# Optimization experiments

Hardware: AMD Instinct MI355X
Metric: run time of the kernel (lower is better)

## Reference

```python
import jax, jax.numpy as jnp
import numpy as np

B, S, D, E, H, K = 2, 2048, 1024, 8, 4096, 2


def setup_inputs() -> dict:
    key = jax.random.key(0)
    ks = jax.random.split(key, 7)
    sd = 1.0 / np.sqrt(D)
    sh = 1.0 / np.sqrt(H)
    return {
        "x": jax.random.normal(ks[0], (B, S, D), dtype=jnp.float32),
        "router_w": jax.random.uniform(ks[1], (D, E), jnp.float32, -sd, sd),
        "router_b": jnp.zeros((E,), jnp.float32),
        "w1": jax.random.uniform(ks[2], (E, D, H), jnp.float32, -sd, sd),
        "b1": jnp.zeros((E, H), jnp.float32),
        "w2": jax.random.uniform(ks[3], (E, H, D), jnp.float32, -sh, sh),
        "b2": jnp.zeros((E, D), jnp.float32),
    }


def reference(x, router_w, router_b, w1, b1, w2, b2):
    # Router: softmax over experts, then top-k and renormalize
    router_logits = jnp.einsum("bsd,de->bse", x, router_w) + router_b
    router_probs = jax.nn.softmax(router_logits, axis=-1)
    top_k_probs, top_k_indices = jax.lax.top_k(router_probs, K)  # [B,S,K]
    top_k_probs = top_k_probs / jnp.sum(top_k_probs, axis=-1, keepdims=True)

    # Dense all-expert FFN (Block assumed: Linear -> GELU -> Linear)
    h = jax.nn.gelu(jnp.einsum("bsd,edh->bseh", x, w1) + b1)  # [B,S,E,H]
    expert_outputs = jnp.einsum("bseh,ehd->bsed", h, w2) + b2  # [B,S,E,D]

    # Gather top-k experts per token and combine with renormalized probs
    idx = top_k_indices[..., None]  # [B,S,K,1]
    selected = jnp.take_along_axis(expert_outputs, idx, axis=2)  # [B,S,K,D]
    return jnp.sum(selected * top_k_probs[..., None], axis=2)  # [B,S,D]
```

## Files before the change

kernel.cpp:

```cpp
#include <hip/hip_runtime.h>
#include <hip/hip_bf16.h>

#define TOK   4096
#define DDIM  1024
#define NEXP  8
#define HDIM  4096
#define KSEL  2
#define NPAIR (TOK * KSEL)
#define NSPLIT 4

typedef __attribute__((ext_vector_type(8))) _Float16 f16x8;
typedef __attribute__((ext_vector_type(4))) _Float16 f16x4;
typedef __attribute__((ext_vector_type(4))) float    f32x4;

__device__ __forceinline__ void gload16(const void* g, void* l) {
  __builtin_amdgcn_global_load_lds((const __attribute__((address_space(1))) void*)g,
                                   (__attribute__((address_space(3))) void*)l, 16, 0, 0);
}

__device__ __forceinline__ float gelu_tanh(float u) {
  float inner = 0.7978845608028654f * (u + 0.044715f * u * u * u);
  float t2 = __expf(2.f * inner);
  return u - u / (t2 + 1.f);
}

__global__ __launch_bounds__(256) void k_router(const float* __restrict__ x,
    const float* __restrict__ rw, const float* __restrict__ rb,
    int* __restrict__ tidx, float* __restrict__ tw,
    _Float16* __restrict__ xb) {
  const int t    = blockIdx.x * 4 + (threadIdx.x >> 6);
  const int lane = threadIdx.x & 63;
  const float* xr = x + (size_t)t * DDIM;
  _Float16*   xbr = xb + (size_t)t * DDIM;
  float acc[NEXP];
#pragma unroll
  for (int e = 0; e < NEXP; ++e) acc[e] = 0.f;
  for (int d0 = lane * 4; d0 < DDIM; d0 += 256) {
    const float4 xv = *(const float4*)(xr + d0);
    f16x4 hx;
    hx[0] = (_Float16)xv.x; hx[1] = (_Float16)xv.y;
    hx[2] = (_Float16)xv.z; hx[3] = (_Float16)xv.w;
    *(f16x4*)(xbr + d0) = hx;
#pragma unroll
    for (int i = 0; i < 4; ++i) {
      const float xs = (&xv.x)[i];
      const float4 r0 = *(const float4*)(rw + (size_t)(d0 + i) * NEXP);
      const float4 r1 = *(const float4*)(rw + (size_t)(d0 + i) * NEXP + 4);
      acc[0] += xs * r0.x; acc[1] += xs * r0.y; acc[2] += xs * r0.z; acc[3] += xs * r0.w;
      acc[4] += xs * r1.x; acc[5] += xs * r1.y; acc[6] += xs * r1.z; acc[7] += xs * r1.w;
    }
  }
#pragma unroll
  for (int e = 0; e < NEXP; ++e) {
    float v = acc[e];
#pragma unroll
    for (int s = 32; s; s >>= 1) v += __shfl_xor(v, s, 64);
    acc[e] = v;
  }
  if (lane == 0) {
    float lg[NEXP];
#pragma unroll
    for (int e = 0; e < NEXP; ++e) lg[e] = acc[e] + rb[e];
    int i0 = 0;
#pragma unroll
    for (int e = 1; e < NEXP; ++e) if (lg[e] > lg[i0]) i0 = e;
    int i1 = -1; float best = -3.4e38f;
#pragma unroll
    for (int e = 0; e < NEXP; ++e) {
      if (e == i0) continue;
      if (lg[e] > best) { best = lg[e]; i1 = e; }
    }
    float w0 = 1.f / (1.f + expf(lg[i1] - lg[i0]));
    tidx[t * 2]     = i0;  tidx[t * 2 + 1] = i1;
    tw[t * 2]       = w0;  tw[t * 2 + 1]   = 1.f - w0;
  }
}

__global__ __launch_bounds__(1024) void k_scan(const int* __restrict__ tidx,
                       const float* __restrict__ tw,
                       int* __restrict__ offs,
                       int* __restrict__ row_token, float* __restrict__ row_w,
                       int* __restrict__ inv) {
  __shared__ int hist[NEXP];
  __shared__ int soff[NEXP + 1];
  __shared__ int scur[NEXP];
  if (threadIdx.x < NEXP) hist[threadIdx.x] = 0;
  __syncthreads();
  const int lane = threadIdx.x & 63;
  int e_loc[NPAIR / 1024];
#pragma unroll
  for (int it = 0; it < NPAIR / 1024; ++it) {
    const int p = it * 1024 + threadIdx.x;
    const int e = tidx[p];
    e_loc[it] = e;
#pragma unroll
    for (int ee = 0; ee < NEXP; ++ee) {
      unsigned long long m = __ballot(e == ee);
      if (m && lane == 0) atomicAdd(&hist[ee], __popcll(m));
    }
  }
  __syncthreads();
  if (threadIdx.x == 0) {
    int run = 0;
    for (int e = 0; e < NEXP; ++e) { soff[e] = run; scur[e] = run; run += hist[e]; }
    soff[NEXP] = run;
    for (int e = 0; e <= NEXP; ++e) offs[e] = soff[e];
  }
  __syncthreads();
#pragma unroll
  for (int it = 0; it < NPAIR / 1024; ++it) {
    const int p = it * 1024 + threadIdx.x;
    const int e = e_loc[it];
    int pos = 0;
#pragma unroll
    for (int ee = 0; ee < NEXP; ++ee) {
      unsigned long long m = __ballot(e == ee);
      if (!m) continue;
      int base = 0;
      if (lane == 0) base = atomicAdd(&scur[ee], __popcll(m));
      base = __shfl(base, 0, 64);
      if (e == ee) pos = base + __popcll(m & ((1ull << lane) - 1ull));
    }
    row_token[pos] = p >> 1;
    row_w[pos]     = tw[p];
    inv[p]         = pos;
  }
}

__global__ __launch_bounds__(256) void k_transpose(const float* __restrict__ in,
    _Float16* __restrict__ out, int Rr, int Cc) {
  __shared__ _Float16 tile[64][72];
  const size_t esz = (size_t)Rr * Cc;
  const float* ip = in + esz * blockIdx.z;
  _Float16*    op = out + esz * blockIdx.z;
  const int i0 = blockIdx.y * 64;
  const int j0 = blockIdx.x * 64;
  const int tx = threadIdx.x & 15, ty = threadIdx.x >> 4;
#pragma unroll
  for (int rr = 0; rr < 4; ++rr) {
    int r = ty + rr * 16;
    float4 v = *(const float4*)(ip + (size_t)(i0 + r) * Cc + j0 + tx * 4);
    tile[r][tx * 4 + 0] = (_Float16)v.x;
    tile[r][tx * 4 + 1] = (_Float16)v.y;
    tile[r][tx * 4 + 2] = (_Float16)v.z;
    tile[r][tx * 4 + 3] = (_Float16)v.w;
  }
  __syncthreads();
#pragma unroll
  for (int cc = 0; cc < 4; ++cc) {
    int c = ty + cc * 16;
    f16x4 o;
#pragma unroll
    for (int k = 0; k < 4; ++k) o[k] = tile[tx * 4 + k][c];
    *(f16x4*)(op + (size_t)(j0 + c) * Rr + i0 + tx * 4) = o;
  }
}

#define BM 128
#define BN 128
#define BKK 32


__global__ __launch_bounds__(256) void k_gemm1(
    const _Float16* __restrict__ xb,
    const _Float16* __restrict__ w1t,
    const float* __restrict__ b1,
    const int* __restrict__ offs,
    const int* __restrict__ row_token,
    _Float16* __restrict__ hbuf) {
  const int e    = blockIdx.z;
  const int off0 = offs[e];
  const int ne   = offs[e + 1] - off0;
  const int m0   = blockIdx.y * BM;
  if (m0 >= ne) return;
  const int n0   = blockIdx.x * BN;
  const int mrem = ne - m0;

  __shared__ __align__(16) char smem[32768];

  const int tid = threadIdx.x;
  const int wv = tid >> 6, lane = tid & 63;
  const int l15 = lane & 15;
  const int wr = wv >> 1, wc = wv & 1;

  const int rA0 = (wv * 2 + 0) * 16 + (lane >> 2);
  const int rA1 = (wv * 2 + 1) * 16 + (lane >> 2);
  const char* a_c = (const char*)xb;
  const char* b_c = (const char*)(w1t + (size_t)e * HDIM * DDIM);
  const int rc0 = (rA0 < mrem) ? rA0 : (mrem - 1);
  const int rc1 = (rA1 < mrem) ? rA1 : (mrem - 1);
  const char* ap0 = a_c + (size_t)row_token[off0 + m0 + rc0] * (DDIM * 2)
                        + (((lane & 3) ^ ((rA0 >> 1) & 3)) << 4);
  const char* ap1 = a_c + (size_t)row_token[off0 + m0 + rc1] * (DDIM * 2)
                        + (((lane & 3) ^ ((rA1 >> 1) & 3)) << 4);
  const char* bp0 = b_c + (size_t)(n0 + rA0) * (DDIM * 2)
                        + (((lane & 3) ^ ((rA0 >> 1) & 3)) << 4);
  const char* bp1 = b_c + (size_t)(n0 + rA1) * (DDIM * 2)
                        + (((lane & 3) ^ ((rA1 >> 1) & 3)) << 4);
  char* ldsA0 = smem + (wv * 2 + 0) * 1024;
  char* ldsA1 = smem + (wv * 2 + 1) * 1024;
  char* ldsB0 = smem + 16384 + (wv * 2 + 0) * 1024;
  char* ldsB1 = smem + 16384 + (wv * 2 + 1) * 1024;

  const unsigned foff = (unsigned)(((lane >> 4) ^ ((l15 >> 1) & 3)) << 4);

  f32x4 acc[4][4] = {};
  const int NT = DDIM / BKK;

  gload16(ap0, ldsA0); gload16(ap1, ldsA1);
  gload16(bp0, ldsB0); gload16(bp1, ldsB1);

#pragma unroll 2
  for (int ks = 0; ks < NT; ++ks) {
    const int cur = ks & 1;
    if (ks + 1 < NT) {
      const int nb = (cur ^ 1) * 8192;
      const size_t kb = (size_t)(ks + 1) * 64;
      gload16(ap0 + kb, ldsA0 + nb); gload16(ap1 + kb, ldsA1 + nb);
      gload16(bp0 + kb, ldsB0 + nb); gload16(bp1 + kb, ldsB1 + nb);
      asm volatile("s_waitcnt vmcnt(4)" ::: "memory");
    } else {
      asm volatile("s_waitcnt vmcnt(0)" ::: "memory");
    }
    __builtin_amdgcn_sched_barrier(0);
    __builtin_amdgcn_s_barrier();
    const char* Ab = smem + cur * 8192;
    const char* Bb = smem + 16384 + cur * 8192;
    f16x8 af[4], bfr[4];
#pragma unroll
    for (int m = 0; m < 4; ++m)
      af[m] = *(const f16x8*)(Ab + (wr * 64 + m * 16 + l15) * 64 + foff);
#pragma unroll
    for (int n = 0; n < 4; ++n)
      bfr[n] = *(const f16x8*)(Bb + (wc * 64 + n * 16 + l15) * 64 + foff);
#pragma unroll
    for (int m = 0; m < 4; ++m)
#pragma unroll
      for (int n = 0; n < 4; ++n)
        acc[m][n] = __builtin_amdgcn_mfma_f32_16x16x32_f16(af[m], bfr[n], acc[m][n], 0, 0, 0);
    __builtin_amdgcn_sched_barrier(0);
    __builtin_amdgcn_s_barrier();
  }

  float bias[4];
#pragma unroll
  for (int n = 0; n < 4; ++n)
    bias[n] = b1[(size_t)e * HDIM + n0 + wc * 64 + n * 16 + l15];
#pragma unroll
  for (int m = 0; m < 4; ++m) {
#pragma unroll
    for (int j = 0; j < 4; ++j) {
      int row = wr * 64 + m * 16 + (lane >> 4) * 4 + j;
#pragma unroll
      for (int n = 0; n < 4; ++n) {
        int col = wc * 64 + n * 16 + l15;
        *(_Float16*)(smem + (row << 8) + (((col << 1) ^ ((row & 15) << 4)))) =
            (_Float16)gelu_tanh(acc[m][n][j] + bias[n]);
      }
    }
  }
  __syncthreads();
  {
    const int srow = tid >> 1, half = tid & 1;
    if (srow < mrem) {
      _Float16* hr = hbuf + (size_t)(off0 + m0 + srow) * HDIM + n0 + half * 64;
#pragma unroll
      for (int i = 0; i < 8; ++i) {
        f16x8 v = *(const f16x8*)(smem + (srow << 8) + (((half * 128 + i * 16) ^ ((srow & 15) << 4))));
        *(f16x8*)(hr + i * 8) = v;
      }
    }
  }
}

template <bool YB>
__global__ __launch_bounds__(256) void k_gemm2(
    const _Float16* __restrict__ hbuf,
    const _Float16* __restrict__ w2t,
    const float* __restrict__ b2,
    const int* __restrict__ offs,
    const int* __restrict__ row_token,
    const float* __restrict__ row_w,
    _Float16* __restrict__ yb,
    float* __restrict__ out) {
  const int zz = blockIdx.z;
  const int e  = zz >> 2;
  const int kh = zz & 3;
  const int off0 = offs[e];
  const int ne   = offs[e + 1] - off0;
  const int m0   = blockIdx.y * BM;
  if (m0 >= ne) return;
  const int n0   = blockIdx.x * BN;
  const int mrem = ne - m0;

  __shared__ __align__(16) char smem[32768];

  const int tid = threadIdx.x;
  const int wv = tid >> 6, lane = tid & 63;
  const int l15 = lane & 15;
  const int wr = wv >> 1, wc = wv & 1;

  const int rA0 = (wv * 2 + 0) * 16 + (lane >> 2);
  const int rA1 = (wv * 2 + 1) * 16 + (lane >> 2);
  const char* a_c = (const char*)hbuf;
  const char* b_c = (const char*)(w2t + (size_t)e * DDIM * HDIM);
  const int rc0 = (rA0 < mrem) ? rA0 : (mrem - 1);
  const int rc1 = (rA1 < mrem) ? rA1 : (mrem - 1);
  const size_t khb = (size_t)kh * ((HDIM / NSPLIT) * 2);
  const char* ap0 = a_c + (size_t)(off0 + m0 + rc0) * (HDIM * 2) + khb
                        + (((lane & 3) ^ ((rA0 >> 1) & 3)) << 4);
  const char* ap1 = a_c + (size_t)(off0 + m0 + rc1) * (HDIM * 2) + khb
                        + (((lane & 3) ^ ((rA1 >> 1) & 3)) << 4);
  const char* bp0 = b_c + (size_t)(n0 + rA0) * (HDIM * 2) + khb
                        + (((lane & 3) ^ ((rA0 >> 1) & 3)) << 4);
  const char* bp1 = b_c + (size_t)(n0 + rA1) * (HDIM * 2) + khb
                        + (((lane & 3) ^ ((rA1 >> 1) & 3)) << 4);
  char* ldsA0 = smem + (wv * 2 + 0) * 1024;
  char* ldsA1 = smem + (wv * 2 + 1) * 1024;
  char* ldsB0 = smem + 16384 + (wv * 2 + 0) * 1024;
  char* ldsB1 = smem + 16384 + (wv * 2 + 1) * 1024;

  const unsigned foff = (unsigned)(((lane >> 4) ^ ((l15 >> 1) & 3)) << 4);

  f32x4 acc[4][4] = {};
  const int NT = (HDIM / NSPLIT) / BKK;

  gload16(ap0, ldsA0); gload16(ap1, ldsA1);
  gload16(bp0, ldsB0); gload16(bp1, ldsB1);

#pragma unroll 2
  for (int ks = 0; ks < NT; ++ks) {
    const int cur = ks & 1;
    if (ks + 1 < NT) {
      const int nb = (cur ^ 1) * 8192;
      const size_t kb = (size_t)(ks + 1) * 64;
      gload16(ap0 + kb, ldsA0 + nb); gload16(ap1 + kb, ldsA1 + nb);
      gload16(bp0 + kb, ldsB0 + nb); gload16(bp1 + kb, ldsB1 + nb);
      asm volatile("s_waitcnt vmcnt(4)" ::: "memory");
    } else {
      asm volatile("s_waitcnt vmcnt(0)" ::: "memory");
    }
    __builtin_amdgcn_sched_barrier(0);
    __builtin_amdgcn_s_barrier();
    const char* Ab = smem + cur * 8192;
    const char* Bb = smem + 16384 + cur * 8192;
    f16x8 af[4], bfr[4];
#pragma unroll
    for (int m = 0; m < 4; ++m)
      af[m] = *(const f16x8*)(Ab + (wr * 64 + m * 16 + l15) * 64 + foff);
#pragma unroll
    for (int n = 0; n < 4; ++n)
      bfr[n] = *(const f16x8*)(Bb + (wc * 64 + n * 16 + l15) * 64 + foff);
#pragma unroll
    for (int m = 0; m < 4; ++m)
#pragma unroll
      for (int n = 0; n < 4; ++n)
        acc[m][n] = __builtin_amdgcn_mfma_f32_16x16x32_f16(af[m], bfr[n], acc[m][n], 0, 0, 0);
    __builtin_amdgcn_sched_barrier(0);
    __builtin_amdgcn_s_barrier();
  }

  if (YB) {
    _Float16* ypart = yb + (size_t)kh * NPAIR * DDIM;
#pragma unroll
    for (int m = 0; m < 4; ++m) {
#pragma unroll
      for (int j = 0; j < 4; ++j) {
        int row = wr * 64 + m * 16 + (lane >> 4) * 4 + j;
#pragma unroll
        for (int n = 0; n < 4; ++n) {
          int col = wc * 64 + n * 16 + l15;
          *(_Float16*)(smem + (row << 8) + (((col << 1) ^ ((row & 15) << 4)))) =
              (_Float16)acc[m][n][j];
        }
      }
    }
    __syncthreads();
    const int srow = tid >> 1, half = tid & 1;
    if (srow < mrem) {
      _Float16* yr = ypart + (size_t)(off0 + m0 + srow) * DDIM + n0 + half * 64;
#pragma unroll
      for (int i = 0; i < 8; ++i) {
        f16x8 v = *(const f16x8*)(smem + (srow << 8) + (((half * 128 + i * 16) ^ ((srow & 15) << 4))));
        *(f16x8*)(yr + i * 8) = v;
      }
    }
  } else {
    float bias[4];
#pragma unroll
    for (int n = 0; n < 4; ++n)
      bias[n] = (kh == 0) ? b2[(size_t)e * DDIM + n0 + wc * 64 + n * 16 + l15] : 0.f;
#pragma unroll
    for (int m = 0; m < 4; ++m) {
#pragma unroll
      for (int j = 0; j < 4; ++j) {
        int row = wr * 64 + m * 16 + (lane >> 4) * 4 + j;
        if (row < mrem) {
          int g = off0 + m0 + row;
          float wgt = row_w[g];
          float* op = out + (size_t)row_token[g] * DDIM + n0 + wc * 64 + l15;
#pragma unroll
          for (int n = 0; n < 4; ++n)
            atomicAdd(op + n * 16, wgt * (acc[m][n][j] + bias[n]));
        }
      }
    }
  }
}

__global__ __launch_bounds__(256) void k_combine(const _Float16* __restrict__ yb,
    const int* __restrict__ inv, const int* __restrict__ tidx,
    const float* __restrict__ tw, const float* __restrict__ b2,
    float* __restrict__ out) {
  const int t  = blockIdx.x * 2 + (threadIdx.x >> 7);
  const int c8 = (threadIdx.x & 127) * 8;
  const int g0 = inv[2 * t],  g1 = inv[2 * t + 1];
  const int e0 = tidx[2 * t], e1 = tidx[2 * t + 1];
  const float w0 = tw[2 * t], w1 = tw[2 * t + 1];
  float s0[8] = {0,0,0,0,0,0,0,0}, s1[8] = {0,0,0,0,0,0,0,0};
#pragma unroll
  for (int p = 0; p < NSPLIT; ++p) {
    const _Float16* yp = yb + (size_t)p * NPAIR * DDIM;
    f16x8 a = *(const f16x8*)(yp + (size_t)g0 * DDIM + c8);
    f16x8 b = *(const f16x8*)(yp + (size_t)g1 * DDIM + c8);
#pragma unroll
    for (int i = 0; i < 8; ++i) { s0[i] += (float)a[i]; s1[i] += (float)b[i]; }
  }
  float o[8];
#pragma unroll
  for (int i = 0; i < 8; ++i) {
    float bA = b2[(size_t)e0 * DDIM + c8 + i];
    float bB = b2[(size_t)e1 * DDIM + c8 + i];
    o[i] = w0 * (s0[i] + bA) + w1 * (s1[i] + bB);
  }
  float* op = out + (size_t)t * DDIM + c8;
  *(float4*)op       = make_float4(o[0], o[1], o[2], o[3]);
  *(float4*)(op + 4) = make_float4(o[4], o[5], o[6], o[7]);
}

extern "C" void kernel_launch(void* const* d_in, const int* in_sizes, int n_in,
                              void* d_out, int out_size, void* d_ws, size_t ws_size,
                              hipStream_t stream) {
  const float* x  = (const float*)d_in[0];
  const float* rw = (const float*)d_in[1];
  const float* rb = (const float*)d_in[2];
  const float* w1 = (const float*)d_in[3];
  const float* b1 = (const float*)d_in[4];
  const float* w2 = (const float*)d_in[5];
  const float* b2 = (const float*)d_in[6];
  float* out = (float*)d_out;
  char* ws = (char*)d_ws;

  int*      tidx    = (int*)(ws + 0);
  float*    tw      = (float*)(ws + 32768);
  int*      offs    = (int*)(ws + 65792);
  int*      row_tok = (int*)(ws + 66048);
  float*    row_w   = (float*)(ws + 98816);
  int*      inv     = (int*)(ws + 131584);
  _Float16* xb      = (_Float16*)(ws + 164352);
  _Float16* wt      = (_Float16*)(ws + 8552960);
  _Float16* hb      = (_Float16*)(ws + 75661824);
  _Float16* yb      = (_Float16*)(ws + 142770688);
  const bool big = ws_size >= 209879552ULL;

  if (!big) hipMemsetAsync(out, 0, (size_t)TOK * DDIM * sizeof(float), stream);

  k_router<<<dim3(TOK / 4), 256, 0, stream>>>(x, rw, rb, tidx, tw, xb);
  k_scan<<<dim3(1), 1024, 0, stream>>>(tidx, tw, offs, row_tok, row_w, inv);
  k_transpose<<<dim3(HDIM / 64, DDIM / 64, NEXP), 256, 0, stream>>>(w1, wt, DDIM, HDIM);
  k_gemm1<<<dim3(HDIM / BN, TOK / BM, NEXP), 256, 0, stream>>>(xb, wt, b1, offs, row_tok, hb);
  k_transpose<<<dim3(DDIM / 64, HDIM / 64, NEXP), 256, 0, stream>>>(w2, wt, HDIM, DDIM);
  if (big) {
    k_gemm2<true><<<dim3(DDIM / BN, TOK / BM, NEXP * NSPLIT), 256, 0, stream>>>(
        hb, wt, b2, offs, row_tok, row_w, yb, out);
    k_combine<<<dim3(TOK / 2), 256, 0, stream>>>(yb, inv, tidx, tw, b2, out);
  } else {
    k_gemm2<false><<<dim3(DDIM / BN, TOK / BM, NEXP * NSPLIT), 256, 0, stream>>>(
        hb, wt, b2, offs, row_tok, row_w, yb, out);
  }
}
```

Baseline: 352.1 us.

## Fuse both weight transposes into one launch and restructure GEMM load waits

Merges the two weight transpose/convert kernels into a single launch that covers w1 and w2, using separate workspace buffers. The intermediate y buffer now reuses the w1t region. This removes one kernel launch and the serialization between transposing w2 and running gemm1. In both GEMM main loops, the wait on the prefetch loads moves from before the MFMA compute to after it, with a full vmcnt(0) drain, so the next tile's global-to-LDS loads overlap the current compute. The catch is that every iteration now fully drains outstanding loads at the barrier.

```diff
diff --git a/kernel.cpp b/kernel.cpp
--- a/kernel.cpp
+++ b/kernel.cpp
@@ -127,14 +127,20 @@
   }
 }
 
-__global__ __launch_bounds__(256) void k_transpose(const float* __restrict__ in,
-    _Float16* __restrict__ out, int Rr, int Cc) {
+__global__ __launch_bounds__(256) void k_transpose2(const float* __restrict__ w1,
+    const float* __restrict__ w2, _Float16* __restrict__ w1t, _Float16* __restrict__ w2t) {
   __shared__ _Float16 tile[64][72];
-  const size_t esz = (size_t)Rr * Cc;
-  const float* ip = in + esz * blockIdx.z;
-  _Float16*    op = out + esz * blockIdx.z;
-  const int i0 = blockIdx.y * 64;
-  const int j0 = blockIdx.x * 64;
+  const int zz = blockIdx.y;
+  const float* ip; _Float16* op; int Rr, Cc, i0, j0;
+  if (zz < NEXP) {
+    ip = w1 + (size_t)zz * DDIM * HDIM;  op = w1t + (size_t)zz * DDIM * HDIM;
+    Rr = DDIM; Cc = HDIM;
+    i0 = (blockIdx.x >> 6) * 64; j0 = (blockIdx.x & 63) * 64;
+  } else {
+    ip = w2 + (size_t)(zz - NEXP) * HDIM * DDIM;  op = w2t + (size_t)(zz - NEXP) * HDIM * DDIM;
+    Rr = HDIM; Cc = DDIM;
+    i0 = (blockIdx.x >> 4) * 64; j0 = (blockIdx.x & 15) * 64;
+  }
   const int tx = threadIdx.x & 15, ty = threadIdx.x >> 4;
 #pragma unroll
   for (int rr = 0; rr < 4; ++rr) {
@@ -209,6 +215,8 @@
 
   gload16(ap0, ldsA0); gload16(ap1, ldsA1);
   gload16(bp0, ldsB0); gload16(bp1, ldsB1);
+  asm volatile("s_waitcnt vmcnt(0)" ::: "memory");
+  __builtin_amdgcn_s_barrier();
 
 #pragma unroll 2
   for (int ks = 0; ks < NT; ++ks) {
@@ -218,12 +226,7 @@
       const size_t kb = (size_t)(ks + 1) * 64;
       gload16(ap0 + kb, ldsA0 + nb); gload16(ap1 + kb, ldsA1 + nb);
       gload16(bp0 + kb, ldsB0 + nb); gload16(bp1 + kb, ldsB1 + nb);
-      asm volatile("s_waitcnt vmcnt(4)" ::: "memory");
-    } else {
-      asm volatile("s_waitcnt vmcnt(0)" ::: "memory");
-    }
-    __builtin_amdgcn_sched_barrier(0);
-    __builtin_amdgcn_s_barrier();
+    }
     const char* Ab = smem + cur * 8192;
     const char* Bb = smem + 16384 + cur * 8192;
     f16x8 af[4], bfr[4];
@@ -239,6 +242,7 @@
       for (int n = 0; n < 4; ++n)
         acc[m][n] = __builtin_amdgcn_mfma_f32_16x16x32_f16(af[m], bfr[n], acc[m][n], 0, 0, 0);
     __builtin_amdgcn_sched_barrier(0);
+    asm volatile("s_waitcnt vmcnt(0)" ::: "memory");
     __builtin_amdgcn_s_barrier();
   }
 
@@ -327,6 +331,8 @@
 
   gload16(ap0, ldsA0); gload16(ap1, ldsA1);
   gload16(bp0, ldsB0); gload16(bp1, ldsB1);
+  asm volatile("s_waitcnt vmcnt(0)" ::: "memory");
+  __builtin_amdgcn_s_barrier();
 
 #pragma unroll 2
   for (int ks = 0; ks < NT; ++ks) {
@@ -336,12 +342,7 @@
       const size_t kb = (size_t)(ks + 1) * 64;
       gload16(ap0 + kb, ldsA0 + nb); gload16(ap1 + kb, ldsA1 + nb);
       gload16(bp0 + kb, ldsB0 + nb); gload16(bp1 + kb, ldsB1 + nb);
-      asm volatile("s_waitcnt vmcnt(4)" ::: "memory");
-    } else {
-      asm volatile("s_waitcnt vmcnt(0)" ::: "memory");
-    }
-    __builtin_amdgcn_sched_barrier(0);
-    __builtin_amdgcn_s_barrier();
+    }
     const char* Ab = smem + cur * 8192;
     const char* Bb = smem + 16384 + cur * 8192;
     f16x8 af[4], bfr[4];
@@ -357,6 +358,7 @@
       for (int n = 0; n < 4; ++n)
         acc[m][n] = __builtin_amdgcn_mfma_f32_16x16x32_f16(af[m], bfr[n], acc[m][n], 0, 0, 0);
     __builtin_amdgcn_sched_barrier(0);
+    asm volatile("s_waitcnt vmcnt(0)" ::: "memory");
     __builtin_amdgcn_s_barrier();
   }
 
@@ -458,24 +460,24 @@
   float*    row_w   = (float*)(ws + 98816);
   int*      inv     = (int*)(ws + 131584);
   _Float16* xb      = (_Float16*)(ws + 164352);
-  _Float16* wt      = (_Float16*)(ws + 8552960);
-  _Float16* hb      = (_Float16*)(ws + 75661824);
-  _Float16* yb      = (_Float16*)(ws + 142770688);
+  _Float16* wtA     = (_Float16*)(ws + 8552960);
+  _Float16* wtB     = (_Float16*)(ws + 75661824);
+  _Float16* hb      = (_Float16*)(ws + 142770688);
+  _Float16* yb      = wtA;
   const bool big = ws_size >= 209879552ULL;
 
   if (!big) hipMemsetAsync(out, 0, (size_t)TOK * DDIM * sizeof(float), stream);
 
   k_router<<<dim3(TOK / 4), 256, 0, stream>>>(x, rw, rb, tidx, tw, xb);
   k_scan<<<dim3(1), 1024, 0, stream>>>(tidx, tw, offs, row_tok, row_w, inv);
-  k_transpose<<<dim3(HDIM / 64, DDIM / 64, NEXP), 256, 0, stream>>>(w1, wt, DDIM, HDIM);
-  k_gemm1<<<dim3(HDIM / BN, TOK / BM, NEXP), 256, 0, stream>>>(xb, wt, b1, offs, row_tok, hb);
-  k_transpose<<<dim3(DDIM / 64, HDIM / 64, NEXP), 256, 0, stream>>>(w2, wt, HDIM, DDIM);
+  k_transpose2<<<dim3(1024, 2 * NEXP), 256, 0, stream>>>(w1, w2, wtA, wtB);
+  k_gemm1<<<dim3(HDIM / BN, TOK / BM, NEXP), 256, 0, stream>>>(xb, wtA, b1, offs, row_tok, hb);
   if (big) {
     k_gemm2<true><<<dim3(DDIM / BN, TOK / BM, NEXP * NSPLIT), 256, 0, stream>>>(
-        hb, wt, b2, offs, row_tok, row_w, yb, out);
+        hb, wtB, b2, offs, row_tok, row_w, yb, out);
     k_combine<<<dim3(TOK / 2), 256, 0, stream>>>(yb, inv, tidx, tw, b2, out);
   } else {
     k_gemm2<false><<<dim3(DDIM / BN, TOK / BM, NEXP * NSPLIT), 256, 0, stream>>>(
-        hb, wt, b2, offs, row_tok, row_w, yb, out);
-  }
-}
+        hb, wtB, b2, offs, row_tok, row_w, yb, out);
+  }
+}
```

New measurement: 385.5 us. 9.5% more time.
